# Optimization experiments

Measured on AMD Instinct MI355X. Metric: run time of the kernel, lower is better.

Reference implementation:

```python
import jax, jax.numpy as jnp
import numpy as np

N_USERS = 50000
N_DISHES = 10000
N_EDGES = 200000
D_IN = 1024
HID = 256
OUT = 128


def _dense_params(key, d_in, d_out):
    kw, kb = jax.random.split(key)
    W = jax.random.normal(kw, (d_in, d_out), jnp.float32) * (1.0 / np.sqrt(d_in))
    b = jnp.zeros((d_out,), jnp.float32)
    return W, b


def setup_inputs() -> dict:
    key = jax.random.key(0)
    ks = jax.random.split(key, 12)
    inp = {
        "user_feat": jax.random.normal(ks[0], (N_USERS, D_IN), jnp.float32),
        "dish_feat": jax.random.normal(ks[1], (N_DISHES, D_IN), jnp.float32),
        "edge_user": jax.random.randint(ks[2], (N_EDGES,), 0, N_USERS, jnp.int32),
        "edge_dish": jax.random.randint(ks[3], (N_EDGES,), 0, N_DISHES, jnp.int32),
    }
    inp["W_ui"], inp["b_ui"] = _dense_params(ks[4], D_IN, HID)   # user_initial_proj
    inp["W_di"], inp["b_di"] = _dense_params(ks[5], D_IN, HID)   # dish_initial_proj
    inp["W_um"], inp["b_um"] = _dense_params(ks[6], D_IN, HID)   # user_message_fn (sender=dish)
    inp["W_dm"], inp["b_dm"] = _dense_params(ks[7], D_IN, HID)   # dish_message_fn (sender=user)
    inp["W_uu"], inp["b_uu"] = _dense_params(ks[8], HID, HID)    # user_update_fn
    inp["W_du"], inp["b_du"] = _dense_params(ks[9], HID, HID)    # dish_update_fn
    inp["W_up"], inp["b_up"] = _dense_params(ks[10], HID, OUT)   # user_proj
    inp["W_dp"], inp["b_dp"] = _dense_params(ks[11], HID, OUT)   # dish_proj
    return inp


def reference(user_feat, dish_feat, edge_user, edge_dish,
              W_ui, b_ui, W_di, b_di, W_um, b_um, W_dm, b_dm,
              W_uu, b_uu, W_du, b_du, W_up, b_up, W_dp, b_dp):
    # initial projections
    user_init = jax.nn.relu(user_feat @ W_ui + b_ui)   # [U, H]
    dish_init = jax.nn.relu(dish_feat @ W_di + b_di)   # [D, H]

    # SimpleConv on 'interacts_reverse': sender=dish, receiver=user
    u_msg = jax.nn.relu(dish_feat[edge_dish] @ W_um + b_um)          # [E, H]
    user_agg = jax.ops.segment_sum(u_msg, edge_user, num_segments=N_USERS)
    user_upd = jax.nn.relu((user_agg + user_init) @ W_uu + b_uu)
    user_emb = user_upd @ W_up + b_up                                 # [U, OUT]

    # SimpleConv on 'interacts': sender=user, receiver=dish
    d_msg = jax.nn.relu(user_feat[edge_user] @ W_dm + b_dm)          # [E, H]
    dish_agg = jax.ops.segment_sum(d_msg, edge_dish, num_segments=N_DISHES)
    dish_upd = jax.nn.relu((dish_agg + dish_init) @ W_du + b_du)
    dish_emb = dish_upd @ W_dp + b_dp                                 # [D, OUT]

    return (user_emb, dish_emb)
```

## Files before the change

### kernel.cpp

```cpp
#include <hip/hip_runtime.h>
#include <hip/hip_bf16.h>

#define D_IN  1024
#define HID   256
#define OUT_D 128

using bf16x8  = __attribute__((ext_vector_type(8))) short;
using bf16x4  = __attribute__((ext_vector_type(4))) short;
using f32x4   = __attribute__((ext_vector_type(4))) float;
typedef unsigned int u32;

__device__ inline float bf2f(short s) {
    unsigned u = ((unsigned)(unsigned short)s) << 16;
    return __uint_as_float(u);
}
__device__ inline short f2bf(float f) {
    __hip_bfloat16 h = __float2bfloat16(f);
    return *reinterpret_cast<short*>(&h);
}

__device__ __forceinline__ void gld16(void* lds, const void* g) {
    __builtin_amdgcn_global_load_lds(
        (const __attribute__((address_space(1))) u32*)g,
        (__attribute__((address_space(3))) u32*)lds, 16, 0, 0);
}

__global__ void pack_all(
    const float* __restrict__ W_ui, const float* __restrict__ W_dm,
    const float* __restrict__ W_di, const float* __restrict__ W_um,
    const float* __restrict__ W_uu, const float* __restrict__ W_du,
    const float* __restrict__ W_up, const float* __restrict__ W_dp,
    const float* __restrict__ b_ui, const float* __restrict__ b_dm,
    const float* __restrict__ b_di, const float* __restrict__ b_um,
    short* __restrict__ Wut, short* __restrict__ Wdt,
    short* __restrict__ Wuut, short* __restrict__ Wdut,
    short* __restrict__ Wupt, short* __restrict__ Wdpt,
    float* __restrict__ bu, float* __restrict__ bd)
{
    const int z = blockIdx.z;
    const int tx = threadIdx.x, ty = threadIdx.y;
    if (z == 8) {
        if (blockIdx.x != 0 || blockIdx.y != 0) return;
        int t = ty * 32 + tx;
        bu[t] = b_ui[t]; bu[256 + t] = b_dm[t];
        bd[t] = b_di[t]; bd[256 + t] = b_um[t];
        return;
    }
    const float* in; short* out; int K, N, n_off = 0;
    switch (z) {
        case 0: in = W_ui; out = Wut;  K = 1024; N = 256; n_off = 0;   break;
        case 1: in = W_dm; out = Wut;  K = 1024; N = 256; n_off = 256; break;
        case 2: in = W_di; out = Wdt;  K = 1024; N = 256; n_off = 0;   break;
        case 3: in = W_um; out = Wdt;  K = 1024; N = 256; n_off = 256; break;
        case 4: in = W_uu; out = Wuut; K = 256;  N = 256; break;
        case 5: in = W_du; out = Wdut; K = 256;  N = 256; break;
        case 6: in = W_up; out = Wupt; K = 256;  N = 128; break;
        default:in = W_dp; out = Wdpt; K = 256;  N = 128; break;
    }
    const int n0 = blockIdx.x * 32, k0 = blockIdx.y * 32;
    if (n0 >= N || k0 >= K) return;
    __shared__ float t[32][33];
#pragma unroll
    for (int j = 0; j < 32; j += 8)
        t[ty + j][tx] = in[(size_t)(k0 + ty + j) * N + (n0 + tx)];
    __syncthreads();
#pragma unroll
    for (int j = 0; j < 32; j += 8)
        out[(size_t)(n_off + n0 + ty + j) * K + (k0 + tx)] = f2bf(t[tx][ty + j]);
}

template <bool RELU, bool AF32, bool CF32>
__global__ __launch_bounds__(256) void mfma_gemm_bf16(
    const void* __restrict__ A, int lda,
    const short* __restrict__ Wt,
    const float* __restrict__ bias,
    void* __restrict__ Cvoid, int M, int N, int K, int nN)
{
    constexpr int BK = 32;
    constexpr int ABYTES = AF32 ? (128 * BK * 4) : (128 * BK * 2);
    constexpr int BBYTES = 128 * BK * 2;
    constexpr int STEP = ABYTES + BBYTES;
    __shared__ __align__(16) char smem[2 * STEP];

    const int tid = threadIdx.x;

    const int nwg = gridDim.x;
    const int orig = blockIdx.x;
    const int qq = nwg >> 3, rr = nwg & 7;
    const int xcd = orig & 7, pos = orig >> 3;
    const int wg = (xcd < rr) ? (xcd * (qq + 1) + pos)
                              : (rr * (qq + 1) + (xcd - rr) * qq + pos);
    const int n0 = (wg % nN) * 128;
    const int m0 = (wg / nN) * 128;

    const int w = tid >> 6, l = tid & 63;
    const int wm = (w >> 1) * 64, wn = (w & 1) * 64;
    const int fr = l & 15, fg = l >> 4;

    f32x4 acc[4][4] = {};

    const char* Abase = (const char*)A;
    const char* Bbase = (const char*)Wt;
    const size_t lda_b = (size_t)lda * (AF32 ? 4 : 2);
    const size_t ldb_b = (size_t)K * 2;

    auto stage = [&](int buf, int k0) {
        char* As = smem + buf * STEP;
        char* Bs = As + ABYTES;
        if constexpr (AF32) {
#pragma unroll
            for (int i = 0; i < 4; ++i) {
                int o = i * 4096 + tid * 16;
                int row = o >> 7, cb = o & 127;
                int scb = cb ^ ((row & 7) << 4);
                int arow = m0 + row; if (arow > M - 1) arow = M - 1;
                gld16(As + o, Abase + (size_t)arow * lda_b + (size_t)k0 * 4 + scb);
            }
        } else {
#pragma unroll
            for (int i = 0; i < 2; ++i) {
                int o = i * 4096 + tid * 16;
                int row = o >> 6, cb = o & 63;
                int scb = cb ^ ((row & 3) << 4);
                int arow = m0 + row; if (arow > M - 1) arow = M - 1;
                gld16(As + o, Abase + (size_t)arow * lda_b + (size_t)k0 * 2 + scb);
            }
        }
#pragma unroll
        for (int i = 0; i < 2; ++i) {
            int o = i * 4096 + tid * 16;
            int row = o >> 6, cb = o & 63;
            int scb = cb ^ ((row & 3) << 4);
            gld16(Bs + o, Bbase + (size_t)(n0 + row) * ldb_b + (size_t)k0 * 2 + scb);
        }
    };

    stage(0, 0);
    __syncthreads();

    int cur = 0;
    for (int k0 = 0; k0 < K; k0 += BK) {
        if (k0 + BK < K) stage(cur ^ 1, k0 + BK);

        const char* As = smem + cur * STEP;
        const char* Bs = As + ABYTES;
        bf16x8 af[4], bfv[4];
#pragma unroll
        for (int i = 0; i < 4; ++i) {
            int row = wm + i * 16 + fr;
            if constexpr (AF32) {
                int sw = (row & 7) << 4;
                const char* rb = As + row * 128;
                f32x4 lo = *reinterpret_cast<const f32x4*>(rb + ((fg * 32) ^ sw));
                f32x4 hi = *reinterpret_cast<const f32x4*>(rb + ((fg * 32 + 16) ^ sw));
                bf16x8 t;
                t[0] = f2bf(lo[0]); t[1] = f2bf(lo[1]);
                t[2] = f2bf(lo[2]); t[3] = f2bf(lo[3]);
                t[4] = f2bf(hi[0]); t[5] = f2bf(hi[1]);
                t[6] = f2bf(hi[2]); t[7] = f2bf(hi[3]);
                af[i] = t;
            } else {
                int cb = (fg * 16) ^ ((row & 3) << 4);
                af[i] = *reinterpret_cast<const bf16x8*>(As + row * 64 + cb);
            }
        }
#pragma unroll
        for (int j = 0; j < 4; ++j) {
            int row = wn + j * 16 + fr;
            int cb = (fg * 16) ^ ((row & 3) << 4);
            bfv[j] = *reinterpret_cast<const bf16x8*>(Bs + row * 64 + cb);
        }
#pragma unroll
        for (int i = 0; i < 4; ++i)
#pragma unroll
            for (int j = 0; j < 4; ++j)
                acc[i][j] = __builtin_amdgcn_mfma_f32_16x16x32_bf16(
                    af[i], bfv[j], acc[i][j], 0, 0, 0);

        __syncthreads();
        cur ^= 1;
    }

#pragma unroll
    for (int i = 0; i < 4; ++i) {
#pragma unroll
        for (int e = 0; e < 4; ++e) {
            int gm = m0 + wm + i * 16 + fg * 4 + e;
            if (gm >= M) continue;
#pragma unroll
            for (int j = 0; j < 4; ++j) {
                int gn = n0 + wn + j * 16 + fr;
                float v = acc[i][j][e] + bias[gn];
                if (RELU) v = fmaxf(v, 0.f);
                if (CF32) ((float*)Cvoid)[(size_t)gm * N + gn] = v;
                else      ((short*)Cvoid)[(size_t)gm * N + gn] = f2bf(v);
            }
        }
    }
}

__global__ void hist2(const int* __restrict__ eu, const int* __restrict__ ed,
                      int* __restrict__ cu, int* __restrict__ cd, int E)
{
    int i = blockIdx.x * blockDim.x + threadIdx.x;
    if (i < E) atomicAdd(&cu[eu[i]], 1);
    else if (i < 2 * E) atomicAdd(&cd[ed[i - E]], 1);
}

__global__ __launch_bounds__(1024) void scan2(
    const int* __restrict__ cnt_u, int* __restrict__ offs_u, int U,
    const int* __restrict__ cnt_d, int* __restrict__ offs_d, int D)
{
    const int* cnt = (blockIdx.x == 0) ? cnt_u : cnt_d;
    int* offs      = (blockIdx.x == 0) ? offs_u : offs_d;
    const int n    = (blockIdx.x == 0) ? U : D;

    __shared__ int tsum[1024];
    const int t = threadIdx.x;
    const int chunk = (n + 1023) / 1024;
    const int lo = t * chunk;
    const int hi = min(lo + chunk, n);
    int s = 0;
    for (int i = lo; i < hi; ++i) s += cnt[i];
    tsum[t] = s;
    __syncthreads();
    for (int d = 1; d < 1024; d <<= 1) {
        int v = (t >= d) ? tsum[t - d] : 0;
        __syncthreads();
        tsum[t] += v;
        __syncthreads();
    }
    int run = (t > 0) ? tsum[t - 1] : 0;
    for (int i = lo; i < hi; ++i) {
        offs[i] = run;
        run += cnt[i];
    }
}

__global__ void fill2(const int* __restrict__ eu, const int* __restrict__ ed,
                      int* __restrict__ offs_u, int* __restrict__ srcl_u,
                      int* __restrict__ offs_d, int* __restrict__ srcl_d, int E)
{
    int i = blockIdx.x * blockDim.x + threadIdx.x;
    if (i < E) {
        int p = atomicAdd(&offs_u[eu[i]], 1);
        srcl_u[p] = ed[i];
    } else if (i < 2 * E) {
        int k = i - E;
        int p = atomicAdd(&offs_d[ed[k]], 1);
        srcl_d[p] = eu[k];
    }
}

__global__ __launch_bounds__(256) void seg_sum_both(
    const short* __restrict__ dish_msg, const short* __restrict__ user_msg,
    const int* __restrict__ srcl_u, const int* __restrict__ offs_u,
    const int* __restrict__ cnt_u,
    const int* __restrict__ srcl_d, const int* __restrict__ offs_d,
    const int* __restrict__ cnt_d,
    short* __restrict__ user_buf, short* __restrict__ dish_buf,
    int U, int D, int nbU)
{
    const short* msg; const int *sl, *oe, *ct; short* acc; int nRows, rb;
    if (blockIdx.x < nbU) {
        msg = dish_msg; sl = srcl_u; oe = offs_u; ct = cnt_u;
        acc = user_buf; nRows = U; rb = blockIdx.x;
    } else {
        msg = user_msg; sl = srcl_d; oe = offs_d; ct = cnt_d;
        acc = dish_buf; nRows = D; rb = blockIdx.x - nbU;
    }
    int row = rb * 4 + (threadIdx.x >> 6);
    if (row >= nRows) return;
    const int lane = threadIdx.x & 63;
    const int deg = ct[row];
    if (deg == 0) return;
    const int base = oe[row] - deg;

    float s0 = 0.f, s1 = 0.f, s2 = 0.f, s3 = 0.f;
    int j = 0;
    for (; j + 4 <= deg; j += 4) {
        int i0 = sl[base + j], i1 = sl[base + j + 1];
        int i2 = sl[base + j + 2], i3 = sl[base + j + 3];
        bf16x4 v0 = *(const bf16x4*)&msg[(size_t)i0 * 512 + lane * 4];
        bf16x4 v1 = *(const bf16x4*)&msg[(size_t)i1 * 512 + lane * 4];
        bf16x4 v2 = *(const bf16x4*)&msg[(size_t)i2 * 512 + lane * 4];
        bf16x4 v3 = *(const bf16x4*)&msg[(size_t)i3 * 512 + lane * 4];
        s0 += bf2f(v0[0]) + bf2f(v1[0]) + bf2f(v2[0]) + bf2f(v3[0]);
        s1 += bf2f(v0[1]) + bf2f(v1[1]) + bf2f(v2[1]) + bf2f(v3[1]);
        s2 += bf2f(v0[2]) + bf2f(v1[2]) + bf2f(v2[2]) + bf2f(v3[2]);
        s3 += bf2f(v0[3]) + bf2f(v1[3]) + bf2f(v2[3]) + bf2f(v3[3]);
    }
    for (; j < deg; ++j) {
        int i0 = sl[base + j];
        bf16x4 v = *(const bf16x4*)&msg[(size_t)i0 * 512 + lane * 4];
        s0 += bf2f(v[0]); s1 += bf2f(v[1]); s2 += bf2f(v[2]); s3 += bf2f(v[3]);
    }
    bf16x4 c = *(bf16x4*)&acc[(size_t)row * 512 + lane * 4];
    c[0] = f2bf(bf2f(c[0]) + s0);
    c[1] = f2bf(bf2f(c[1]) + s1);
    c[2] = f2bf(bf2f(c[2]) + s2);
    c[3] = f2bf(bf2f(c[3]) + s3);
    *(bf16x4*)&acc[(size_t)row * 512 + lane * 4] = c;
}

extern "C" void kernel_launch(void* const* d_in, const int* in_sizes, int n_in,
                              void* d_out, int out_size, void* d_ws, size_t ws_size,
                              hipStream_t stream)
{
    const float* user_feat = (const float*)d_in[0];
    const float* dish_feat = (const float*)d_in[1];
    const int*   edge_user = (const int*)d_in[2];
    const int*   edge_dish = (const int*)d_in[3];
    const float* W_ui = (const float*)d_in[4];  const float* b_ui = (const float*)d_in[5];
    const float* W_di = (const float*)d_in[6];  const float* b_di = (const float*)d_in[7];
    const float* W_um = (const float*)d_in[8];  const float* b_um = (const float*)d_in[9];
    const float* W_dm = (const float*)d_in[10]; const float* b_dm = (const float*)d_in[11];
    const float* W_uu = (const float*)d_in[12]; const float* b_uu = (const float*)d_in[13];
    const float* W_du = (const float*)d_in[14]; const float* b_du = (const float*)d_in[15];
    const float* W_up = (const float*)d_in[16]; const float* b_up = (const float*)d_in[17];
    const float* W_dp = (const float*)d_in[18]; const float* b_dp = (const float*)d_in[19];

    const int U = in_sizes[0] / D_IN;
    const int D = in_sizes[1] / D_IN;
    const int E = in_sizes[2];

    float* out = (float*)d_out;
    float* user_emb = out;
    float* dish_emb = out + (size_t)U * OUT_D;

    short* sws = (short*)d_ws;
    short* user_buf = sws;
    short* dish_buf = user_buf + (size_t)U * 512;
    short* user_upd = dish_buf + (size_t)D * 512;
    short* dish_upd = user_upd + (size_t)U * 256;
    short* Wut  = dish_upd + (size_t)D * 256;
    short* Wdt  = Wut  + (size_t)512 * 1024;
    short* Wuut = Wdt  + (size_t)512 * 1024;
    short* Wdut = Wuut + (size_t)256 * 256;
    short* Wupt = Wdut + (size_t)256 * 256;
    short* Wdpt = Wupt + (size_t)128 * 256;
    float* bu   = (float*)(Wdpt + (size_t)128 * 256);
    float* bd   = bu + 512;
    int*   cnt_u  = (int*)(bd + 512);
    int*   cnt_d  = cnt_u + U;
    int*   offs_u = cnt_d + D;
    int*   offs_d = offs_u + U;
    int*   srcl_u = offs_d + D;
    int*   srcl_d = srcl_u + E;

    hipLaunchKernelGGL(pack_all, dim3(8, 32, 9), dim3(32, 8), 0, stream,
                       W_ui, W_dm, W_di, W_um, W_uu, W_du, W_up, W_dp,
                       b_ui, b_dm, b_di, b_um,
                       Wut, Wdt, Wuut, Wdut, Wupt, Wdpt, bu, bd);

    hipMemsetAsync(cnt_u, 0, (size_t)(U + D) * sizeof(int), stream);
    int eg2 = (2 * E + 255) / 256;
    hipLaunchKernelGGL(hist2, dim3(eg2), dim3(256), 0, stream,
                       edge_user, edge_dish, cnt_u, cnt_d, E);
    hipLaunchKernelGGL(scan2, dim3(2), dim3(1024), 0, stream,
                       cnt_u, offs_u, U, cnt_d, offs_d, D);
    hipLaunchKernelGGL(fill2, dim3(eg2), dim3(256), 0, stream,
                       edge_user, edge_dish, offs_u, srcl_u, offs_d, srcl_d, E);

    hipLaunchKernelGGL((mfma_gemm_bf16<true, true, false>),
                       dim3(((U + 127) / 128) * 4), dim3(256), 0, stream,
                       user_feat, D_IN, Wut, bu, user_buf, U, 512, D_IN, 4);
    hipLaunchKernelGGL((mfma_gemm_bf16<true, true, false>),
                       dim3(((D + 127) / 128) * 4), dim3(256), 0, stream,
                       dish_feat, D_IN, Wdt, bd, dish_buf, D, 512, D_IN, 4);

    int nbU = (U + 3) / 4;
    hipLaunchKernelGGL(seg_sum_both, dim3(nbU + (D + 3) / 4), dim3(256), 0, stream,
                       dish_buf + HID, user_buf + HID,
                       srcl_u, offs_u, cnt_u, srcl_d, offs_d, cnt_d,
                       user_buf, dish_buf, U, D, nbU);

    hipLaunchKernelGGL((mfma_gemm_bf16<true, false, false>),
                       dim3(((U + 127) / 128) * 2), dim3(256), 0, stream,
                       user_buf, 512, Wuut, b_uu, user_upd, U, HID, HID, 2);
    hipLaunchKernelGGL((mfma_gemm_bf16<true, false, false>),
                       dim3(((D + 127) / 128) * 2), dim3(256), 0, stream,
                       dish_buf, 512, Wdut, b_du, dish_upd, D, HID, HID, 2);

    hipLaunchKernelGGL((mfma_gemm_bf16<false, false, true>),
                       dim3((U + 127) / 128), dim3(256), 0, stream,
                       user_upd, HID, Wupt, b_up, user_emb, U, OUT_D, HID, 1);
    hipLaunchKernelGGL((mfma_gemm_bf16<false, false, true>),
                       dim3((D + 127) / 128), dim3(256), 0, stream,
                       dish_upd, HID, Wdpt, b_dp, dish_emb, D, OUT_D, HID, 1);
}
```

Measured before the change: 395.1 us.

## Batch user and dish GEMMs into single launches and drop LDS double buffering

Merges each pair of user/dish GEMM launches into one grid that picks its problem from the block index. This removes three launches and lets the small dish GEMM share the device with the user GEMM instead of running alone on an underfilled grid. It also replaces the double-buffered LDS pipeline with a single buffer and a sync after each load. That halves LDS use, which may raise occupancy, but global loads no longer overlap the MFMA work.

```diff
diff --git a/kernel.cpp b/kernel.cpp
--- a/kernel.cpp
+++ b/kernel.cpp
@@ -70,22 +70,33 @@
 }
 
 template <bool RELU, bool AF32, bool CF32>
-__global__ __launch_bounds__(256) void mfma_gemm_bf16(
-    const void* __restrict__ A, int lda,
-    const short* __restrict__ Wt,
-    const float* __restrict__ bias,
-    void* __restrict__ Cvoid, int M, int N, int K, int nN)
-{
-    constexpr int BK = 32;
-    constexpr int ABYTES = AF32 ? (128 * BK * 4) : (128 * BK * 2);
-    constexpr int BBYTES = 128 * BK * 2;
-    constexpr int STEP = ABYTES + BBYTES;
-    __shared__ __align__(16) char smem[2 * STEP];
+__global__ __launch_bounds__(256) void mfma_gemm2(
+    const void* __restrict__ A0_, int lda0, const short* __restrict__ Wt0,
+    const float* __restrict__ bias0, void* __restrict__ C0,
+    int M0, int N0, int K0, int nN0, int nb0,
+    const void* __restrict__ A1_, int lda1, const short* __restrict__ Wt1,
+    const float* __restrict__ bias1, void* __restrict__ C1,
+    int M1, int N1, int K1, int nN1)
+{
+    constexpr int ABYTES = AF32 ? 16384 : 8192;
+    constexpr int BBYTES = 8192;
+    __shared__ __align__(16) char smem[ABYTES + BBYTES];
+    char* As = smem;
+    char* Bs = smem + ABYTES;
 
     const int tid = threadIdx.x;
 
-    const int nwg = gridDim.x;
-    const int orig = blockIdx.x;
+    const void* A_; const short* Wt; const float* bias; void* Cv;
+    int lda, M, N, K, nN, nwg, orig;
+    if ((int)blockIdx.x < nb0) {
+        A_ = A0_; lda = lda0; Wt = Wt0; bias = bias0; Cv = C0;
+        M = M0; N = N0; K = K0; nN = nN0; nwg = nb0; orig = blockIdx.x;
+    } else {
+        A_ = A1_; lda = lda1; Wt = Wt1; bias = bias1; Cv = C1;
+        M = M1; N = N1; K = K1; nN = nN1;
+        nwg = gridDim.x - nb0; orig = blockIdx.x - nb0;
+    }
+
     const int qq = nwg >> 3, rr = nwg & 7;
     const int xcd = orig & 7, pos = orig >> 3;
     const int wg = (xcd < rr) ? (xcd * (qq + 1) + pos)
@@ -99,14 +110,12 @@
 
     f32x4 acc[4][4] = {};
 
-    const char* Abase = (const char*)A;
-    const char* Bbase = (const char*)Wt;
+    const char* Ab = (const char*)A_;
+    const char* Bb = (const char*)Wt;
     const size_t lda_b = (size_t)lda * (AF32 ? 4 : 2);
     const size_t ldb_b = (size_t)K * 2;
 
-    auto stage = [&](int buf, int k0) {
-        char* As = smem + buf * STEP;
-        char* Bs = As + ABYTES;
+    for (int k0 = 0; k0 < K; k0 += 32) {
         if constexpr (AF32) {
 #pragma unroll
             for (int i = 0; i < 4; ++i) {
@@ -114,7 +123,7 @@
                 int row = o >> 7, cb = o & 127;
                 int scb = cb ^ ((row & 7) << 4);
                 int arow = m0 + row; if (arow > M - 1) arow = M - 1;
-                gld16(As + o, Abase + (size_t)arow * lda_b + (size_t)k0 * 4 + scb);
+                gld16(As + o, Ab + (size_t)arow * lda_b + (size_t)k0 * 4 + scb);
             }
         } else {
 #pragma unroll
@@ -123,7 +132,7 @@
                 int row = o >> 6, cb = o & 63;
                 int scb = cb ^ ((row & 3) << 4);
                 int arow = m0 + row; if (arow > M - 1) arow = M - 1;
-                gld16(As + o, Abase + (size_t)arow * lda_b + (size_t)k0 * 2 + scb);
+                gld16(As + o, Ab + (size_t)arow * lda_b + (size_t)k0 * 2 + scb);
             }
         }
 #pragma unroll
@@ -131,19 +140,10 @@
             int o = i * 4096 + tid * 16;
             int row = o >> 6, cb = o & 63;
             int scb = cb ^ ((row & 3) << 4);
-            gld16(Bs + o, Bbase + (size_t)(n0 + row) * ldb_b + (size_t)k0 * 2 + scb);
-        }
-    };
-
-    stage(0, 0);
-    __syncthreads();
-
-    int cur = 0;
-    for (int k0 = 0; k0 < K; k0 += BK) {
-        if (k0 + BK < K) stage(cur ^ 1, k0 + BK);
-
-        const char* As = smem + cur * STEP;
-        const char* Bs = As + ABYTES;
+            gld16(Bs + o, Bb + (size_t)(n0 + row) * ldb_b + (size_t)k0 * 2 + scb);
+        }
+        __syncthreads();
+
         bf16x8 af[4], bfv[4];
 #pragma unroll
         for (int i = 0; i < 4; ++i) {
@@ -178,7 +178,6 @@
                     af[i], bfv[j], acc[i][j], 0, 0, 0);
 
         __syncthreads();
-        cur ^= 1;
     }
 
 #pragma unroll
@@ -192,8 +191,8 @@
                 int gn = n0 + wn + j * 16 + fr;
                 float v = acc[i][j][e] + bias[gn];
                 if (RELU) v = fmaxf(v, 0.f);
-                if (CF32) ((float*)Cvoid)[(size_t)gm * N + gn] = v;
-                else      ((short*)Cvoid)[(size_t)gm * N + gn] = f2bf(v);
+                if (CF32) ((float*)Cv)[(size_t)gm * N + gn] = v;
+                else      ((short*)Cv)[(size_t)gm * N + gn] = f2bf(v);
             }
         }
     }
@@ -362,12 +361,16 @@
     hipLaunchKernelGGL(fill2, dim3(eg2), dim3(256), 0, stream,
                        edge_user, edge_dish, offs_u, srcl_u, offs_d, srcl_d, E);
 
-    hipLaunchKernelGGL((mfma_gemm_bf16<true, true, false>),
-                       dim3(((U + 127) / 128) * 4), dim3(256), 0, stream,
-                       user_feat, D_IN, Wut, bu, user_buf, U, 512, D_IN, 4);
-    hipLaunchKernelGGL((mfma_gemm_bf16<true, true, false>),
-                       dim3(((D + 127) / 128) * 4), dim3(256), 0, stream,
-                       dish_feat, D_IN, Wdt, bd, dish_buf, D, 512, D_IN, 4);
+    const int nbU128 = (U + 127) / 128;
+    const int nbD128 = (D + 127) / 128;
+
+    {
+        int nb0 = nbU128 * 4, nb1 = nbD128 * 4;
+        hipLaunchKernelGGL((mfma_gemm2<true, true, false>),
+                           dim3(nb0 + nb1), dim3(256), 0, stream,
+                           user_feat, D_IN, Wut, bu, user_buf, U, 512, D_IN, 4, nb0,
+                           dish_feat, D_IN, Wdt, bd, dish_buf, D, 512, D_IN, 4);
+    }
 
     int nbU = (U + 3) / 4;
     hipLaunchKernelGGL(seg_sum_both, dim3(nbU + (D + 3) / 4), dim3(256), 0, stream,
@@ -375,17 +378,19 @@
                        srcl_u, offs_u, cnt_u, srcl_d, offs_d, cnt_d,
                        user_buf, dish_buf, U, D, nbU);
 
-    hipLaunchKernelGGL((mfma_gemm_bf16<true, false, false>),
-                       dim3(((U + 127) / 128) * 2), dim3(256), 0, stream,
-                       user_buf, 512, Wuut, b_uu, user_upd, U, HID, HID, 2);
-    hipLaunchKernelGGL((mfma_gemm_bf16<true, false, false>),
-                       dim3(((D + 127) / 128) * 2), dim3(256), 0, stream,
-                       dish_buf, 512, Wdut, b_du, dish_upd, D, HID, HID, 2);
-
-    hipLaunchKernelGGL((mfma_gemm_bf16<false, false, true>),
-                       dim3((U + 127) / 128), dim3(256), 0, stream,
-                       user_upd, HID, Wupt, b_up, user_emb, U, OUT_D, HID, 1);
-    hipLaunchKernelGGL((mfma_gemm_bf16<false, false, true>),
-                       dim3((D + 127) / 128), dim3(256), 0, stream,
-                       dish_upd, HID, Wdpt, b_dp, dish_emb, D, OUT_D, HID, 1);
-}
+    {
+        int nb0 = nbU128 * 2, nb1 = nbD128 * 2;
+        hipLaunchKernelGGL((mfma_gemm2<true, false, false>),
+                           dim3(nb0 + nb1), dim3(256), 0, stream,
+                           user_buf, 512, Wuut, b_uu, user_upd, U, HID, HID, 2, nb0,
+                           dish_buf, 512, Wdut, b_du, dish_upd, D, HID, HID, 2);
+    }
+
+    {
+        int nb0 = nbU128, nb1 = nbD128;
+        hipLaunchKernelGGL((mfma_gemm2<false, false, true>),
+                           dim3(nb0 + nb1), dim3(256), 0, stream,
+                           user_upd, HID, Wupt, b_up, user_emb, U, OUT_D, HID, 1, nb0,
+                           dish_upd, HID, Wdpt, b_dp, dish_emb, D, OUT_D, HID, 1);
+    }
+}
```

New measurement: 353.2 us. -10.6%, faster.
